# Performance work log

Hardware: AMD Instinct MI355X
Metric: run time of the kernel (lower is better)

Reference implementation:

```python
import jax, jax.numpy as jnp
import numpy as np

N_NODES = 100000
N_EDGES = 1600000
N_GRAPHS = 1024
F_IN = 128
H = 64


def setup_inputs() -> dict:
    key = jax.random.key(0)
    ks = jax.random.split(key, 12)
    x = jax.random.normal(ks[0], (N_NODES, F_IN), dtype=jnp.float32)
    edge_index = jax.random.randint(ks[1], (2, N_EDGES), 0, N_NODES, dtype=jnp.int64)
    edge_attr = jax.random.normal(ks[2], (N_EDGES, 4), dtype=jnp.float32)
    batch = jnp.sort(jax.random.randint(ks[3], (N_NODES,), 0, N_GRAPHS, dtype=jnp.int64))
    def glorot(k, fan_in, fan_out):
        s = jnp.sqrt(6.0 / (fan_in + fan_out))
        return jax.random.uniform(k, (fan_in, fan_out), jnp.float32, -s, s)
    return {
        "x": x, "edge_index": edge_index, "edge_attr": edge_attr, "batch": batch,
        "W1": glorot(ks[4], F_IN, H), "b1": jnp.zeros((H,), jnp.float32),
        "W2": glorot(ks[5], H, H),    "b2": jnp.zeros((H,), jnp.float32),
        "W3": glorot(ks[6], H, H),    "b3": jnp.zeros((H,), jnp.float32),
        "lin_w": glorot(ks[7], H, 1), "lin_b": jnp.zeros((1,), jnp.float32),
    }


def _gcn_layer(h, src, dst, norm, W, b):
    # GCNConv: out_i = sum_{j in N(i) u {i}} norm_ij * (x_j W) + b
    hw = h @ W                               # [N, H]
    msg = hw[src] * norm[:, None]            # [E+N, H] gather + scale
    out = jax.ops.segment_sum(msg, dst, num_segments=N_NODES)
    return out + b


def reference(x, edge_index, edge_attr, batch, W1, b1, W2, b2, W3, b3, lin_w, lin_b):
    # add self-loops (PyG GCNConv default) and symmetric normalization
    loop = jnp.arange(N_NODES, dtype=edge_index.dtype)
    src = jnp.concatenate([edge_index[0], loop])   # [E+N]
    dst = jnp.concatenate([edge_index[1], loop])
    deg = jax.ops.segment_sum(jnp.ones_like(src, dtype=x.dtype), dst,
                              num_segments=N_NODES)  # >=1 thanks to self-loops
    dinv = jax.lax.rsqrt(deg)
    norm = dinv[src] * dinv[dst]                    # [E+N]

    h = jax.nn.relu(_gcn_layer(x, src, dst, norm, W1, b1))
    h = jax.nn.relu(_gcn_layer(h, src, dst, norm, W2, b2))
    h = _gcn_layer(h, src, dst, norm, W3, b3)        # no relu after conv3 (as in source)

    # global mean pool over graphs
    sums = jax.ops.segment_sum(h, batch, num_segments=N_GRAPHS)        # [G, H]
    cnts = jax.ops.segment_sum(jnp.ones((N_NODES,), h.dtype), batch,
                               num_segments=N_GRAPHS)
    pooled = sums / jnp.maximum(cnts, 1.0)[:, None]
    # dropout p=0.5 is identity in eval mode (training=False)
    return pooled @ lin_w + lin_b                                       # [G, 1]
```

## Files before the change

kernel.cpp:

```cpp
#include <hip/hip_runtime.h>
#include <hip/hip_fp16.h>

#define N_NODES 100000
#define N_EDGES 1600000
#define N_GRAPHS 1024
#define F_IN 128
#define HDIM 64
#define NCOARSE 391
#define NBLK_AB 1024
#define EPB 1563
#define NH (NCOARSE * 8 * 128)
#define NSCN (NH / 256)

typedef _Float16 half4f __attribute__((ext_vector_type(4)));
typedef float f32x4 __attribute__((ext_vector_type(4)));

__global__ __launch_bounds__(256) void wtilde_k(const float* __restrict__ W3,
                                                const float* __restrict__ b3,
                                                const float* __restrict__ lw,
                                                float* __restrict__ wt,
                                                float* __restrict__ bc,
                                                float* __restrict__ gsum,
                                                float* __restrict__ gcnt) {
    if (blockIdx.x == 0) {
        int t = threadIdx.x;
        if (t < 64) {
            float d = 0.0f;
            for (int c = 0; c < 64; ++c) d = fmaf(W3[t * 64 + c], lw[c], d);
            wt[t] = d;
        } else if (t == 64) {
            float d = 0.0f;
            for (int c = 0; c < 64; ++c) d = fmaf(b3[c], lw[c], d);
            bc[0] = d;
        }
    } else {
        int i = (blockIdx.x - 1) * 256 + threadIdx.x;
        if (i < N_GRAPHS) { gsum[i] = 0.0f; gcnt[i] = 0.0f; }
    }
}

__global__ __launch_bounds__(256) void coarse_hist_k(const int* __restrict__ dst,
                                                     int* __restrict__ H) {
    __shared__ int hist[NCOARSE];
    for (int i = threadIdx.x; i < NCOARSE; i += 256) hist[i] = 0;
    __syncthreads();
    int b = blockIdx.x;
    int e0 = b * EPB, e1 = min(e0 + EPB, N_EDGES);
    for (int e = e0 + threadIdx.x; e < e1; e += 256)
        atomicAdd(&hist[dst[e] >> 8], 1);
    __syncthreads();
    int g = b & 7, j = b >> 3;
    for (int c = threadIdx.x; c < NCOARSE; c += 256)
        H[(c * 8 + g) * 128 + j] = hist[c];
}

__global__ __launch_bounds__(256) void scanA_k(const int* __restrict__ H,
                                               int* __restrict__ bsum) {
    __shared__ int sm[256];
    int i = blockIdx.x * 256 + threadIdx.x;
    sm[threadIdx.x] = H[i];
    __syncthreads();
    for (int o = 128; o > 0; o >>= 1) {
        if (threadIdx.x < o) sm[threadIdx.x] += sm[threadIdx.x + o];
        __syncthreads();
    }
    if (threadIdx.x == 0) bsum[blockIdx.x] = sm[0];
}

__global__ __launch_bounds__(1024) void scanB_k(const int* __restrict__ bsum,
                                                int* __restrict__ boff) {
    __shared__ int tsum[1024];
    int t = threadIdx.x;
    int v[2], s = 0;
#pragma unroll
    for (int j = 0; j < 2; ++j) {
        int idx = t * 2 + j;
        v[j] = (idx < NSCN) ? bsum[idx] : 0;
        s += v[j];
    }
    tsum[t] = s;
    __syncthreads();
    for (int o = 1; o < 1024; o <<= 1) {
        int add = (t >= o) ? tsum[t - o] : 0;
        __syncthreads();
        tsum[t] += add;
        __syncthreads();
    }
    int excl = tsum[t] - s;
#pragma unroll
    for (int j = 0; j < 2; ++j) {
        int idx = t * 2 + j;
        if (idx < NSCN) { boff[idx] = excl; excl += v[j]; }
    }
}

__global__ __launch_bounds__(256) void scanC_k(const int* __restrict__ H,
                                               const int* __restrict__ boff,
                                               int* __restrict__ goff,
                                               int* __restrict__ cbase) {
    __shared__ int sm[256];
    int blk = blockIdx.x, t = threadIdx.x;
    int i = blk * 256 + t;
    int v = H[i];
    sm[t] = v;
    __syncthreads();
    for (int o = 1; o < 256; o <<= 1) {
        int add = (t >= o) ? sm[t - o] : 0;
        __syncthreads();
        sm[t] += add;
        __syncthreads();
    }
    int excl = boff[blk] + sm[t] - v;
    goff[i] = excl;
    if ((i & 1023) == 0) cbase[i >> 10] = excl;
    if (i == 0) cbase[NCOARSE] = N_EDGES;
}

__global__ __launch_bounds__(256) void coarse_scatter_k(const int* __restrict__ src,
                                                        const int* __restrict__ dst,
                                                        const int* __restrict__ goff,
                                                        int* __restrict__ eC) {
    __shared__ int cur[NCOARSE];
    int b = blockIdx.x, t = threadIdx.x, g = b & 7, j = b >> 3;
    for (int c = t; c < NCOARSE; c += 256)
        cur[c] = goff[(c * 8 + g) * 128 + j];
    __syncthreads();
    int e0 = b * EPB, e1 = min(e0 + EPB, N_EDGES);
    for (int e = e0 + t; e < e1; e += 256) {
        int s = src[e], d = dst[e];
        int pos = atomicAdd(&cur[d >> 8], 1);
        eC[pos] = s | ((d & 255) << 17);
    }
}

__global__ __launch_bounds__(1024) void bucket_count_k(const int* __restrict__ eC,
                                                       const int* __restrict__ cbase,
                                                       int* __restrict__ rowptr,
                                                       float* __restrict__ dinv) {
    __shared__ int cnt[256];
    __shared__ int sc[256];
    int c = blockIdx.x, t = threadIdx.x;
    if (t < 256) cnt[t] = 0;
    __syncthreads();
    int s0 = cbase[c], s1 = cbase[c + 1];
    for (int e = s0 + t; e < s1; e += 1024)
        atomicAdd(&cnt[(eC[e] >> 17) & 255], 1);
    __syncthreads();
    if (t < 256) sc[t] = cnt[t];
    __syncthreads();
    for (int o = 1; o < 256; o <<= 1) {
        int add = (t >= o && t < 256) ? sc[t - o] : 0;
        __syncthreads();
        if (t < 256) sc[t] += add;
        __syncthreads();
    }
    int node = c * 256 + t;
    if (t < 256 && node < N_NODES) {
        rowptr[node] = s0 + sc[t] - cnt[t];
        dinv[node] = rsqrtf((float)cnt[t] + 1.0f);
    }
    if (node == N_NODES - 1) rowptr[N_NODES] = s1;
}

__global__ __launch_bounds__(1024) void bucket_scatter_k(const int* __restrict__ eC,
                                                         const int* __restrict__ cbase,
                                                         const int* __restrict__ rowptr,
                                                         const float* __restrict__ dinv,
                                                         int2* __restrict__ epack) {
    __shared__ int cur[256];
    __shared__ float dv[256];
    int c = blockIdx.x, t = threadIdx.x;
    int node = c * 256 + t;
    if (t < 256) {
        cur[t] = (node < N_NODES) ? rowptr[node] : 0;
        dv[t] = (node < N_NODES) ? dinv[node] : 0.0f;
    }
    __syncthreads();
    int s0 = cbase[c], s1 = cbase[c + 1];
    for (int e = s0 + t; e < s1; e += 1024) {
        int u = eC[e];
        int s = u & 0x1FFFF;
        int doff = (u >> 17) & 255;
        float nm = dinv[s] * dv[doff];
        int pos = atomicAdd(&cur[doff], 1);
        epack[pos] = make_int2(s, __float_as_int(nm));
    }
}

template <int K>
__global__ __launch_bounds__(256) void gemm_k(const float* __restrict__ A,
                                              const float* __restrict__ W,
                                              __half* __restrict__ out) {
    constexpr int PITCH = K + 24;
    __shared__ __align__(16) _Float16 Wt[64 * PITCH];
    for (int i = threadIdx.x; i < K * 64; i += 256) {
        int k = i >> 6, c = i & 63;
        Wt[c * PITCH + k] = (_Float16)W[i];
    }
    __syncthreads();

    const int lane = threadIdx.x & 63;
    const int wid  = threadIdx.x >> 6;
    const int cl   = lane & 15;
    const int kq   = lane >> 4;
    const int c0   = wid * 16;
    const int r0   = blockIdx.x * 64;

    f32x4 acc[4] = {};
#pragma unroll
    for (int ks = 0; ks < K / 16; ++ks) {
        const int kbase = ks * 16 + kq * 4;
        const half4f bf = *(const half4f*)&Wt[(c0 + cl) * PITCH + kbase];
#pragma unroll
        for (int m = 0; m < 4; ++m) {
            int r = r0 + m * 16 + cl;
            float4 a4 = (r < N_NODES)
                            ? *(const float4*)(A + (size_t)r * K + kbase)
                            : make_float4(0.f, 0.f, 0.f, 0.f);
            half4f af = {(_Float16)a4.x, (_Float16)a4.y,
                         (_Float16)a4.z, (_Float16)a4.w};
            acc[m] = __builtin_amdgcn_mfma_f32_16x16x16f16(af, bf, acc[m], 0, 0, 0);
        }
    }
#pragma unroll
    for (int m = 0; m < 4; ++m) {
        int rbase = r0 + m * 16 + kq * 4;
#pragma unroll
        for (int reg = 0; reg < 4; ++reg) {
            int r = rbase + reg;
            if (r < N_NODES)
                out[(size_t)r * HDIM + c0 + cl] = __float2half(acc[m][reg]);
        }
    }
}

template <bool RELU_OUT>
__global__ __launch_bounds__(256) void agg_k(const int* __restrict__ rowptr,
                                             const int2* __restrict__ epack,
                                             const float* __restrict__ dinv,
                                             const __half* __restrict__ hw,
                                             const float* __restrict__ b,
                                             float* __restrict__ h) {
    const int lane = threadIdx.x & 63;
    int node = (blockIdx.x * 256 + threadIdx.x) >> 6;
    if (node >= N_NODES) return;
    int e0 = rowptr[node], e1 = rowptr[node + 1];
    float dv = dinv[node];
    float acc = b[lane] + __half2float(hw[(size_t)node * HDIM + lane]) * dv * dv;

    int e = e0;
    if ((e & 1) && e < e1) {
        int2 m = epack[e];
        acc = fmaf(__half2float(hw[(size_t)m.x * HDIM + lane]),
                   __int_as_float(m.y), acc);
        ++e;
    }
    for (; e + 8 <= e1; e += 8) {
        int4 m0 = *(const int4*)(epack + e);
        int4 m1 = *(const int4*)(epack + e + 2);
        int4 m2 = *(const int4*)(epack + e + 4);
        int4 m3 = *(const int4*)(epack + e + 6);
        float v0 = __half2float(hw[(size_t)m0.x * HDIM + lane]);
        float v1 = __half2float(hw[(size_t)m0.z * HDIM + lane]);
        float v2 = __half2float(hw[(size_t)m1.x * HDIM + lane]);
        float v3 = __half2float(hw[(size_t)m1.z * HDIM + lane]);
        float v4 = __half2float(hw[(size_t)m2.x * HDIM + lane]);
        float v5 = __half2float(hw[(size_t)m2.z * HDIM + lane]);
        float v6 = __half2float(hw[(size_t)m3.x * HDIM + lane]);
        float v7 = __half2float(hw[(size_t)m3.z * HDIM + lane]);
        acc = fmaf(v0, __int_as_float(m0.y), acc);
        acc = fmaf(v1, __int_as_float(m0.w), acc);
        acc = fmaf(v2, __int_as_float(m1.y), acc);
        acc = fmaf(v3, __int_as_float(m1.w), acc);
        acc = fmaf(v4, __int_as_float(m2.y), acc);
        acc = fmaf(v5, __int_as_float(m2.w), acc);
        acc = fmaf(v6, __int_as_float(m3.y), acc);
        acc = fmaf(v7, __int_as_float(m3.w), acc);
    }
    for (; e < e1; ++e) {
        int2 m = epack[e];
        acc = fmaf(__half2float(hw[(size_t)m.x * HDIM + lane]),
                   __int_as_float(m.y), acc);
    }
    if (RELU_OUT) acc = fmaxf(acc, 0.0f);
    h[(size_t)node * HDIM + lane] = acc;
}

__global__ __launch_bounds__(256) void s_k(const float* __restrict__ h2r,
                                           const float* __restrict__ wt,
                                           float* __restrict__ s) {
    __shared__ float wl[64];
    if (threadIdx.x < 64) wl[threadIdx.x] = wt[threadIdx.x];
    __syncthreads();
    int i = blockIdx.x * 256 + threadIdx.x;
    if (i >= N_NODES) return;
    const float4* row = (const float4*)(h2r + (size_t)i * HDIM);
    float dot = 0.0f;
#pragma unroll
    for (int q = 0; q < 16; ++q) {
        float4 v = row[q];
        dot = fmaf(v.x, wl[q * 4 + 0], dot);
        dot = fmaf(v.y, wl[q * 4 + 1], dot);
        dot = fmaf(v.z, wl[q * 4 + 2], dot);
        dot = fmaf(v.w, wl[q * 4 + 3], dot);
    }
    s[i] = dot;
}

__global__ __launch_bounds__(256) void agg3s_k(const int* __restrict__ rowptr,
                                               const int2* __restrict__ epack,
                                               const float* __restrict__ dinv,
                                               const float* __restrict__ s,
                                               const int* __restrict__ batch,
                                               const float* __restrict__ bc,
                                               float* __restrict__ gsum,
                                               float* __restrict__ gcnt) {
    int i = blockIdx.x * 256 + threadIdx.x;
    bool act = i < N_NODES;
    float acc = 0.0f;
    int g = -1;
    if (act) {
        g = batch[i];
        float dv = dinv[i];
        acc = bc[0] + dv * dv * s[i];
        int e0 = rowptr[i], e1 = rowptr[i + 1];
        int e = e0;
        for (; e + 4 <= e1; e += 4) {
            int2 m0 = epack[e], m1 = epack[e + 1];
            int2 m2 = epack[e + 2], m3 = epack[e + 3];
            float t0 = s[m0.x], t1 = s[m1.x], t2 = s[m2.x], t3 = s[m3.x];
            acc = fmaf(t0, __int_as_float(m0.y), acc);
            acc = fmaf(t1, __int_as_float(m1.y), acc);
            acc = fmaf(t2, __int_as_float(m2.y), acc);
            acc = fmaf(t3, __int_as_float(m3.y), acc);
        }
        for (; e < e1; ++e) {
            int2 m = epack[e];
            acc = fmaf(s[m.x], __int_as_float(m.y), acc);
        }
    }
    int g0 = __shfl(g, 0);
    bool uni = (__ballot(act && (g == g0)) == ~0ULL);
    if (uni) {
        for (int o = 32; o > 0; o >>= 1) acc += __shfl_down(acc, o);
        if ((threadIdx.x & 63) == 0) {
            atomicAdd(&gsum[g0], acc);
            atomicAdd(&gcnt[g0], 64.0f);
        }
    } else if (act) {
        atomicAdd(&gsum[g], acc);
        atomicAdd(&gcnt[g], 1.0f);
    }
}

__global__ void final_k(float* __restrict__ out, const float* __restrict__ gsum,
                        const float* __restrict__ gcnt, const float* __restrict__ lb) {
    int g = blockIdx.x * blockDim.x + threadIdx.x;
    if (g < N_GRAPHS) out[g] = gsum[g] / fmaxf(gcnt[g], 1.0f) + lb[0];
}

extern "C" void kernel_launch(void* const* d_in, const int* in_sizes, int n_in,
                              void* d_out, int out_size, void* d_ws, size_t ws_size,
                              hipStream_t stream) {
    const float* x     = (const float*)d_in[0];
    const int*   eidx  = (const int*)d_in[1];
    const int*   batch = (const int*)d_in[3];
    const float* W1 = (const float*)d_in[4];
    const float* b1 = (const float*)d_in[5];
    const float* W2 = (const float*)d_in[6];
    const float* b2 = (const float*)d_in[7];
    const float* W3 = (const float*)d_in[8];
    const float* b3 = (const float*)d_in[9];
    const float* lin_w = (const float*)d_in[10];
    const float* lin_b = (const float*)d_in[11];
    float* out = (float*)d_out;

    const int* src = eidx;
    const int* dst = eidx + N_EDGES;

    float*  ws     = (float*)d_ws;
    float*  dinv   = ws;
    int*    rowptr = (int*)(ws + 100352);
    int*    cbase  = rowptr + 100352;
    int*    bsum   = cbase + 512;
    int*    boff   = bsum + 1600;
    int*    H      = boff + 1600;
    int*    goff   = H + 400384;
    int2*   epack  = (int2*)(goff + 400384);
    __half* bufH   = (__half*)(epack + N_EDGES);
    float*  bufF   = (float*)(bufH + 6400000);
    float*  gsum   = bufF + 6400000;
    float*  gcnt   = gsum + 1024;
    float*  wt     = gcnt + 1024;
    float*  bc     = wt + 128;
    float*  s      = bc + 16;
    int*    eC     = (int*)bufH;

    wtilde_k<<<5, 256, 0, stream>>>(W3, b3, lin_w, wt, bc, gsum, gcnt);
    coarse_hist_k<<<NBLK_AB, 256, 0, stream>>>(dst, H);
    scanA_k<<<NSCN, 256, 0, stream>>>(H, bsum);
    scanB_k<<<1, 1024, 0, stream>>>(bsum, boff);
    scanC_k<<<NSCN, 256, 0, stream>>>(H, boff, goff, cbase);
    coarse_scatter_k<<<NBLK_AB, 256, 0, stream>>>(src, dst, goff, eC);
    bucket_count_k<<<NCOARSE, 1024, 0, stream>>>(eC, cbase, rowptr, dinv);
    bucket_scatter_k<<<NCOARSE, 1024, 0, stream>>>(eC, cbase, rowptr, dinv, epack);

    gemm_k<F_IN><<<1563, 256, 0, stream>>>(x, W1, bufH);
    agg_k<true><<<25000, 256, 0, stream>>>(rowptr, epack, dinv, bufH, b1, bufF);

    gemm_k<HDIM><<<1563, 256, 0, stream>>>(bufF, W2, bufH);
    agg_k<true><<<25000, 256, 0, stream>>>(rowptr, epack, dinv, bufH, b2, bufF);

    s_k<<<391, 256, 0, stream>>>(bufF, wt, s);
    agg3s_k<<<391, 256, 0, stream>>>(rowptr, epack, dinv, s, batch, bc, gsum, gcnt);
    final_k<<<(N_GRAPHS + 255) / 256, 256, 0, stream>>>(out, gsum, gcnt, lin_b);
}
```

Baseline: 403.6 us.

## Factor GCN normalization into GEMM output, drop per-edge weights, fuse readout

The symmetric normalization is split into a source-side dinv scale applied in the GEMM epilogue and a destination-side scale applied once after aggregation. This lets the CSR store only 4-byte source indices instead of 8-byte (index, weight) pairs, which halves edge-list traffic in every aggregation pass. The layer-2 aggregation now emits the projected scalar directly, which removes the separate s_k kernel and the bufF write. The layer-3 scalar aggregation splits each node's edges across 4 threads. The coarse histogram and scatter kernels use fewer, larger blocks, giving a smaller histogram and scan.

```diff
diff --git a/kernel.cpp b/kernel.cpp
--- a/kernel.cpp
+++ b/kernel.cpp
@@ -7,9 +7,9 @@
 #define F_IN 128
 #define HDIM 64
 #define NCOARSE 391
-#define NBLK_AB 1024
-#define EPB 1563
-#define NH (NCOARSE * 8 * 128)
+#define NBLK_C 256
+#define EPB 6250
+#define NH (NCOARSE * 256)
 #define NSCN (NH / 256)
 
 typedef _Float16 half4f __attribute__((ext_vector_type(4)));
@@ -39,19 +39,19 @@
     }
 }
 
-__global__ __launch_bounds__(256) void coarse_hist_k(const int* __restrict__ dst,
-                                                     int* __restrict__ H) {
+__global__ __launch_bounds__(1024) void coarse_hist_k(const int* __restrict__ dst,
+                                                      int* __restrict__ H) {
     __shared__ int hist[NCOARSE];
-    for (int i = threadIdx.x; i < NCOARSE; i += 256) hist[i] = 0;
+    for (int i = threadIdx.x; i < NCOARSE; i += 1024) hist[i] = 0;
     __syncthreads();
     int b = blockIdx.x;
-    int e0 = b * EPB, e1 = min(e0 + EPB, N_EDGES);
-    for (int e = e0 + threadIdx.x; e < e1; e += 256)
+    int e0 = b * EPB;
+    for (int e = e0 + threadIdx.x; e < e0 + EPB; e += 1024)
         atomicAdd(&hist[dst[e] >> 8], 1);
     __syncthreads();
     int g = b & 7, j = b >> 3;
-    for (int c = threadIdx.x; c < NCOARSE; c += 256)
-        H[(c * 8 + g) * 128 + j] = hist[c];
+    for (int c = threadIdx.x; c < NCOARSE; c += 1024)
+        H[(c * 8 + g) * 32 + j] = hist[c];
 }
 
 __global__ __launch_bounds__(256) void scanA_k(const int* __restrict__ H,
@@ -71,14 +71,8 @@
                                                 int* __restrict__ boff) {
     __shared__ int tsum[1024];
     int t = threadIdx.x;
-    int v[2], s = 0;
-#pragma unroll
-    for (int j = 0; j < 2; ++j) {
-        int idx = t * 2 + j;
-        v[j] = (idx < NSCN) ? bsum[idx] : 0;
-        s += v[j];
-    }
-    tsum[t] = s;
+    int v = (t < NSCN) ? bsum[t] : 0;
+    tsum[t] = v;
     __syncthreads();
     for (int o = 1; o < 1024; o <<= 1) {
         int add = (t >= o) ? tsum[t - o] : 0;
@@ -86,12 +80,7 @@
         tsum[t] += add;
         __syncthreads();
     }
-    int excl = tsum[t] - s;
-#pragma unroll
-    for (int j = 0; j < 2; ++j) {
-        int idx = t * 2 + j;
-        if (idx < NSCN) { boff[idx] = excl; excl += v[j]; }
-    }
+    if (t < NSCN) boff[t] = tsum[t] - v;
 }
 
 __global__ __launch_bounds__(256) void scanC_k(const int* __restrict__ H,
@@ -112,21 +101,21 @@
     }
     int excl = boff[blk] + sm[t] - v;
     goff[i] = excl;
-    if ((i & 1023) == 0) cbase[i >> 10] = excl;
-    if (i == 0) cbase[NCOARSE] = N_EDGES;
-}
-
-__global__ __launch_bounds__(256) void coarse_scatter_k(const int* __restrict__ src,
-                                                        const int* __restrict__ dst,
-                                                        const int* __restrict__ goff,
-                                                        int* __restrict__ eC) {
+    if (t == 0) cbase[blk] = excl;
+    if (blk == 0 && t == 0) cbase[NCOARSE] = N_EDGES;
+}
+
+__global__ __launch_bounds__(1024) void coarse_scatter_k(const int* __restrict__ src,
+                                                         const int* __restrict__ dst,
+                                                         const int* __restrict__ goff,
+                                                         int* __restrict__ eC) {
     __shared__ int cur[NCOARSE];
     int b = blockIdx.x, t = threadIdx.x, g = b & 7, j = b >> 3;
-    for (int c = t; c < NCOARSE; c += 256)
-        cur[c] = goff[(c * 8 + g) * 128 + j];
-    __syncthreads();
-    int e0 = b * EPB, e1 = min(e0 + EPB, N_EDGES);
-    for (int e = e0 + t; e < e1; e += 256) {
+    for (int c = t; c < NCOARSE; c += 1024)
+        cur[c] = goff[(c * 8 + g) * 32 + j];
+    __syncthreads();
+    int e0 = b * EPB;
+    for (int e = e0 + t; e < e0 + EPB; e += 1024) {
         int s = src[e], d = dst[e];
         int pos = atomicAdd(&cur[d >> 8], 1);
         eC[pos] = s | ((d & 255) << 17);
@@ -165,31 +154,24 @@
 __global__ __launch_bounds__(1024) void bucket_scatter_k(const int* __restrict__ eC,
                                                          const int* __restrict__ cbase,
                                                          const int* __restrict__ rowptr,
-                                                         const float* __restrict__ dinv,
-                                                         int2* __restrict__ epack) {
+                                                         int* __restrict__ es) {
     __shared__ int cur[256];
-    __shared__ float dv[256];
     int c = blockIdx.x, t = threadIdx.x;
     int node = c * 256 + t;
-    if (t < 256) {
-        cur[t] = (node < N_NODES) ? rowptr[node] : 0;
-        dv[t] = (node < N_NODES) ? dinv[node] : 0.0f;
-    }
+    if (t < 256) cur[t] = (node < N_NODES) ? rowptr[node] : 0;
     __syncthreads();
     int s0 = cbase[c], s1 = cbase[c + 1];
     for (int e = s0 + t; e < s1; e += 1024) {
         int u = eC[e];
-        int s = u & 0x1FFFF;
-        int doff = (u >> 17) & 255;
-        float nm = dinv[s] * dv[doff];
-        int pos = atomicAdd(&cur[doff], 1);
-        epack[pos] = make_int2(s, __float_as_int(nm));
+        int pos = atomicAdd(&cur[(u >> 17) & 255], 1);
+        es[pos] = u & 0x1FFFF;
     }
 }
 
 template <int K>
 __global__ __launch_bounds__(256) void gemm_k(const float* __restrict__ A,
                                               const float* __restrict__ W,
+                                              const float* __restrict__ dinv,
                                               __half* __restrict__ out) {
     constexpr int PITCH = K + 24;
     __shared__ __align__(16) _Float16 Wt[64 * PITCH];
@@ -229,127 +211,95 @@
         for (int reg = 0; reg < 4; ++reg) {
             int r = rbase + reg;
             if (r < N_NODES)
-                out[(size_t)r * HDIM + c0 + cl] = __float2half(acc[m][reg]);
+                out[(size_t)r * HDIM + c0 + cl] =
+                    __float2half(acc[m][reg] * dinv[r]);
         }
     }
 }
 
-template <bool RELU_OUT>
+template <bool RELU_OUT, bool EMIT_S>
 __global__ __launch_bounds__(256) void agg_k(const int* __restrict__ rowptr,
-                                             const int2* __restrict__ epack,
+                                             const int* __restrict__ es,
                                              const float* __restrict__ dinv,
                                              const __half* __restrict__ hw,
                                              const float* __restrict__ b,
-                                             float* __restrict__ h) {
+                                             float* __restrict__ h,
+                                             const float* __restrict__ wt,
+                                             float* __restrict__ ss) {
     const int lane = threadIdx.x & 63;
     int node = (blockIdx.x * 256 + threadIdx.x) >> 6;
     if (node >= N_NODES) return;
     int e0 = rowptr[node], e1 = rowptr[node + 1];
     float dv = dinv[node];
-    float acc = b[lane] + __half2float(hw[(size_t)node * HDIM + lane]) * dv * dv;
+    float acc = __half2float(hw[(size_t)node * HDIM + lane]);
 
     int e = e0;
-    if ((e & 1) && e < e1) {
-        int2 m = epack[e];
-        acc = fmaf(__half2float(hw[(size_t)m.x * HDIM + lane]),
-                   __int_as_float(m.y), acc);
+    while ((e & 3) && e < e1) {
+        acc += __half2float(hw[(size_t)es[e] * HDIM + lane]);
         ++e;
     }
     for (; e + 8 <= e1; e += 8) {
-        int4 m0 = *(const int4*)(epack + e);
-        int4 m1 = *(const int4*)(epack + e + 2);
-        int4 m2 = *(const int4*)(epack + e + 4);
-        int4 m3 = *(const int4*)(epack + e + 6);
-        float v0 = __half2float(hw[(size_t)m0.x * HDIM + lane]);
-        float v1 = __half2float(hw[(size_t)m0.z * HDIM + lane]);
-        float v2 = __half2float(hw[(size_t)m1.x * HDIM + lane]);
-        float v3 = __half2float(hw[(size_t)m1.z * HDIM + lane]);
-        float v4 = __half2float(hw[(size_t)m2.x * HDIM + lane]);
-        float v5 = __half2float(hw[(size_t)m2.z * HDIM + lane]);
-        float v6 = __half2float(hw[(size_t)m3.x * HDIM + lane]);
-        float v7 = __half2float(hw[(size_t)m3.z * HDIM + lane]);
-        acc = fmaf(v0, __int_as_float(m0.y), acc);
-        acc = fmaf(v1, __int_as_float(m0.w), acc);
-        acc = fmaf(v2, __int_as_float(m1.y), acc);
-        acc = fmaf(v3, __int_as_float(m1.w), acc);
-        acc = fmaf(v4, __int_as_float(m2.y), acc);
-        acc = fmaf(v5, __int_as_float(m2.w), acc);
-        acc = fmaf(v6, __int_as_float(m3.y), acc);
-        acc = fmaf(v7, __int_as_float(m3.w), acc);
-    }
-    for (; e < e1; ++e) {
-        int2 m = epack[e];
-        acc = fmaf(__half2float(hw[(size_t)m.x * HDIM + lane]),
-                   __int_as_float(m.y), acc);
-    }
+        int4 ma = *(const int4*)(es + e);
+        int4 mb = *(const int4*)(es + e + 4);
+        float v0 = __half2float(hw[(size_t)ma.x * HDIM + lane]);
+        float v1 = __half2float(hw[(size_t)ma.y * HDIM + lane]);
+        float v2 = __half2float(hw[(size_t)ma.z * HDIM + lane]);
+        float v3 = __half2float(hw[(size_t)ma.w * HDIM + lane]);
+        float v4 = __half2float(hw[(size_t)mb.x * HDIM + lane]);
+        float v5 = __half2float(hw[(size_t)mb.y * HDIM + lane]);
+        float v6 = __half2float(hw[(size_t)mb.z * HDIM + lane]);
+        float v7 = __half2float(hw[(size_t)mb.w * HDIM + lane]);
+        acc += v0 + v1 + v2 + v3 + v4 + v5 + v6 + v7;
+    }
+    for (; e < e1; ++e)
+        acc += __half2float(hw[(size_t)es[e] * HDIM + lane]);
+
+    acc = b[lane] + dv * acc;
     if (RELU_OUT) acc = fmaxf(acc, 0.0f);
-    h[(size_t)node * HDIM + lane] = acc;
-}
-
-__global__ __launch_bounds__(256) void s_k(const float* __restrict__ h2r,
-                                           const float* __restrict__ wt,
-                                           float* __restrict__ s) {
-    __shared__ float wl[64];
-    if (threadIdx.x < 64) wl[threadIdx.x] = wt[threadIdx.x];
-    __syncthreads();
-    int i = blockIdx.x * 256 + threadIdx.x;
-    if (i >= N_NODES) return;
-    const float4* row = (const float4*)(h2r + (size_t)i * HDIM);
-    float dot = 0.0f;
-#pragma unroll
-    for (int q = 0; q < 16; ++q) {
-        float4 v = row[q];
-        dot = fmaf(v.x, wl[q * 4 + 0], dot);
-        dot = fmaf(v.y, wl[q * 4 + 1], dot);
-        dot = fmaf(v.z, wl[q * 4 + 2], dot);
-        dot = fmaf(v.w, wl[q * 4 + 3], dot);
-    }
-    s[i] = dot;
+    if constexpr (EMIT_S) {
+        float d = acc * wt[lane];
+        for (int o = 32; o > 0; o >>= 1) d += __shfl_down(d, o);
+        if (lane == 0) ss[node] = d * dv;
+    } else {
+        h[(size_t)node * HDIM + lane] = acc;
+    }
 }
 
 __global__ __launch_bounds__(256) void agg3s_k(const int* __restrict__ rowptr,
-                                               const int2* __restrict__ epack,
+                                               const int* __restrict__ es,
                                                const float* __restrict__ dinv,
-                                               const float* __restrict__ s,
+                                               const float* __restrict__ ss,
                                                const int* __restrict__ batch,
                                                const float* __restrict__ bc,
                                                float* __restrict__ gsum,
                                                float* __restrict__ gcnt) {
-    int i = blockIdx.x * 256 + threadIdx.x;
+    int t = blockIdx.x * 256 + threadIdx.x;
+    int i = t >> 2, q = t & 3;
     bool act = i < N_NODES;
-    float acc = 0.0f;
+    float contrib = 0.0f;
     int g = -1;
     if (act) {
         g = batch[i];
         float dv = dinv[i];
-        acc = bc[0] + dv * dv * s[i];
-        int e0 = rowptr[i], e1 = rowptr[i + 1];
-        int e = e0;
-        for (; e + 4 <= e1; e += 4) {
-            int2 m0 = epack[e], m1 = epack[e + 1];
-            int2 m2 = epack[e + 2], m3 = epack[e + 3];
-            float t0 = s[m0.x], t1 = s[m1.x], t2 = s[m2.x], t3 = s[m3.x];
-            acc = fmaf(t0, __int_as_float(m0.y), acc);
-            acc = fmaf(t1, __int_as_float(m1.y), acc);
-            acc = fmaf(t2, __int_as_float(m2.y), acc);
-            acc = fmaf(t3, __int_as_float(m3.y), acc);
-        }
-        for (; e < e1; ++e) {
-            int2 m = epack[e];
-            acc = fmaf(s[m.x], __int_as_float(m.y), acc);
-        }
+        int e0 = rowptr[i], len = rowptr[i + 1] - e0;
+        int qa = e0 + ((len * q) >> 2);
+        int qb = e0 + ((len * (q + 1)) >> 2);
+        float acc = (q == 0) ? ss[i] : 0.0f;
+#pragma unroll 4
+        for (int e = qa; e < qb; ++e) acc += ss[es[e]];
+        contrib = dv * acc + ((q == 0) ? bc[0] : 0.0f);
     }
     int g0 = __shfl(g, 0);
     bool uni = (__ballot(act && (g == g0)) == ~0ULL);
     if (uni) {
-        for (int o = 32; o > 0; o >>= 1) acc += __shfl_down(acc, o);
+        for (int o = 32; o > 0; o >>= 1) contrib += __shfl_down(contrib, o);
         if ((threadIdx.x & 63) == 0) {
-            atomicAdd(&gsum[g0], acc);
-            atomicAdd(&gcnt[g0], 64.0f);
+            atomicAdd(&gsum[g0], contrib);
+            atomicAdd(&gcnt[g0], 16.0f);
         }
     } else if (act) {
-        atomicAdd(&gsum[g], acc);
-        atomicAdd(&gcnt[g], 1.0f);
+        atomicAdd(&gsum[g], contrib);
+        if (q == 0) atomicAdd(&gcnt[g], 1.0f);
     }
 }
 
@@ -383,35 +333,34 @@
     int*    rowptr = (int*)(ws + 100352);
     int*    cbase  = rowptr + 100352;
     int*    bsum   = cbase + 512;
-    int*    boff   = bsum + 1600;
-    int*    H      = boff + 1600;
-    int*    goff   = H + 400384;
-    int2*   epack  = (int2*)(goff + 400384);
-    __half* bufH   = (__half*)(epack + N_EDGES);
+    int*    boff   = bsum + 512;
+    int*    H      = boff + 512;
+    int*    goff   = H + 100352;
+    int*    es     = goff + 100352;
+    __half* bufH   = (__half*)(es + N_EDGES);
     float*  bufF   = (float*)(bufH + 6400000);
     float*  gsum   = bufF + 6400000;
     float*  gcnt   = gsum + 1024;
     float*  wt     = gcnt + 1024;
     float*  bc     = wt + 128;
-    float*  s      = bc + 16;
+    float*  ss     = bc + 16;
     int*    eC     = (int*)bufH;
 
     wtilde_k<<<5, 256, 0, stream>>>(W3, b3, lin_w, wt, bc, gsum, gcnt);
-    coarse_hist_k<<<NBLK_AB, 256, 0, stream>>>(dst, H);
+    coarse_hist_k<<<NBLK_C, 1024, 0, stream>>>(dst, H);
     scanA_k<<<NSCN, 256, 0, stream>>>(H, bsum);
     scanB_k<<<1, 1024, 0, stream>>>(bsum, boff);
     scanC_k<<<NSCN, 256, 0, stream>>>(H, boff, goff, cbase);
-    coarse_scatter_k<<<NBLK_AB, 256, 0, stream>>>(src, dst, goff, eC);
+    coarse_scatter_k<<<NBLK_C, 1024, 0, stream>>>(src, dst, goff, eC);
     bucket_count_k<<<NCOARSE, 1024, 0, stream>>>(eC, cbase, rowptr, dinv);
-    bucket_scatter_k<<<NCOARSE, 1024, 0, stream>>>(eC, cbase, rowptr, dinv, epack);
-
-    gemm_k<F_IN><<<1563, 256, 0, stream>>>(x, W1, bufH);
-    agg_k<true><<<25000, 256, 0, stream>>>(rowptr, epack, dinv, bufH, b1, bufF);
-
-    gemm_k<HDIM><<<1563, 256, 0, stream>>>(bufF, W2, bufH);
-    agg_k<true><<<25000, 256, 0, stream>>>(rowptr, epack, dinv, bufH, b2, bufF);
-
-    s_k<<<391, 256, 0, stream>>>(bufF, wt, s);
-    agg3s_k<<<391, 256, 0, stream>>>(rowptr, epack, dinv, s, batch, bc, gsum, gcnt);
+    bucket_scatter_k<<<NCOARSE, 1024, 0, stream>>>(eC, cbase, rowptr, es);
+
+    gemm_k<F_IN><<<1563, 256, 0, stream>>>(x, W1, dinv, bufH);
+    agg_k<true, false><<<25000, 256, 0, stream>>>(rowptr, es, dinv, bufH, b1,
+                                                  bufF, nullptr, nullptr);
+    gemm_k<HDIM><<<1563, 256, 0, stream>>>(bufF, W2, dinv, bufH);
+    agg_k<true, true><<<25000, 256, 0, stream>>>(rowptr, es, dinv, bufH, b2,
+                                                 nullptr, wt, ss);
+    agg3s_k<<<1563, 256, 0, stream>>>(rowptr, es, dinv, ss, batch, bc, gsum, gcnt);
     final_k<<<(N_GRAPHS + 255) / 256, 256, 0, stream>>>(out, gsum, gcnt, lin_b);
 }
```

Result: no change. 408.4 us (+1.2%).
